# Kernel optimization log

Hardware: AMD Instinct MI355X
Metric: run time of the kernel (lower is better)

## Reference

```python
import jax, jax.numpy as jnp
import numpy as np
import math

EPS = 1e-5
ANGLES = [0, 30, 45, 60, 90, 135]
SIGMA = 0.3
POOL = 7  # top-hat neighbourhood


def make_masks(H, W):
    # Soft Gaussian stripe masks, one per angle: [A, H, W]
    ys = np.linspace(-1.0, 1.0, H)
    xs = np.linspace(-1.0, 1.0, W)
    gy, gx = np.meshgrid(ys, xs, indexing='ij')
    ms = []
    for a in ANGLES:
        t = a * math.pi / 180.0
        perp = gx * (-math.sin(t)) + gy * math.cos(t)
        ms.append(np.exp(-0.5 * (perp / SIGMA) ** 2))
    return jnp.asarray(np.stack(ms, axis=0), dtype=jnp.float32)


def dwconv1d(x, w):
    # x: [B, C, L], w: [C, 1, K] depthwise, 'same' padding (odd K)
    return jax.lax.conv_general_dilated(
        x, w, window_strides=(1,), padding='SAME',
        feature_group_count=x.shape[1],
        dimension_numbers=('NCH', 'OIH', 'NCH'))


def bn(x, gamma, beta, axes, pshape):
    # Training-mode batch norm (biased variance, as in torch forward)
    mean = x.mean(axes, keepdims=True)
    var = x.var(axes, keepdims=True)
    return (x - mean) * jax.lax.rsqrt(var + EPS) * gamma.reshape(pshape) + beta.reshape(pshape)


def maxpool_same(x, k):
    # torch MaxPool2d(k, stride=1, padding=k//2): pad with -inf
    p = k // 2
    return jax.lax.reduce_window(
        x, -jnp.inf, jax.lax.max,
        window_dimensions=(1, 1, k, k), window_strides=(1, 1, 1, 1),
        padding=[(0, 0), (0, 0), (p, p), (p, p)])


def setup_inputs() -> dict:
    key = jax.random.key(0)
    ks = jax.random.split(key, 8)
    B, C, H, W = 128, 576, 28, 28
    K = 3
    x = jax.random.normal(ks[0], (B, C, H, W), dtype=jnp.float32)
    h_w = jax.random.normal(ks[1], (C, 1, K), dtype=jnp.float32) * 0.2
    v_w = jax.random.normal(ks[2], (C, 1, K), dtype=jnp.float32) * 0.2
    f_w = jax.random.normal(ks[3], (C,), dtype=jnp.float32) * 0.2  # 1x1 dw conv = per-channel scale
    h_g = jnp.ones((C,), jnp.float32); h_b = jnp.zeros((C,), jnp.float32)
    v_g = jnp.ones((C,), jnp.float32); v_b = jnp.zeros((C,), jnp.float32)
    f_g = jnp.ones((C,), jnp.float32); f_b = jnp.zeros((C,), jnp.float32)
    return {"x": x, "h_w": h_w, "h_g": h_g, "h_b": h_b,
            "v_w": v_w, "v_g": v_g, "v_b": v_b,
            "f_w": f_w, "f_g": f_g, "f_b": f_b}


def reference(x, h_w, h_g, h_b, v_w, v_g, v_b, f_w, f_g, f_b):
    B, C, H, W = x.shape
    # Horizontal stream: mean over W -> dw conv1d over H -> BN1d -> sigmoid -> [B,C,H,1]
    ph = x.mean(axis=-1)                                   # [B, C, H]
    A_h = jax.nn.sigmoid(bn(dwconv1d(ph, h_w), h_g, h_b, (0, 2), (1, C, 1)))[..., None]
    # Vertical stream: mean over H -> dw conv1d over W -> BN1d -> sigmoid -> [B,C,1,W]
    pv = x.mean(axis=-2)                                   # [B, C, W]
    A_v = jax.nn.sigmoid(bn(dwconv1d(pv, v_w), v_g, v_b, (0, 2), (1, C, 1)))[:, :, None, :]
    # Focal spot stream: white top-hat -> per-channel scale -> BN2d -> sigmoid
    spots = maxpool_same(x, POOL) - x                      # [B, C, H, W]
    A_f = jax.nn.sigmoid(bn(spots * f_w[None, :, None, None], f_g, f_b, (0, 2, 3), (1, C, 1, 1)))
    # Orientation bank: masked global means, sigmoid per angle, mean over angles
    masks = make_masks(H, W)                               # [A, H, W]
    resp = jnp.einsum('bchw,ahw->bca', x, masks) / (H * W) # [B, C, A]
    A_t = jax.nn.sigmoid(resp).mean(axis=-1)[:, :, None, None]
    return x * A_h * A_v * A_f * A_t
```

## Files before the change

kernel.cpp:

```cpp
#include <hip/hip_runtime.h>
#include <math.h>

#define B 128
#define C 576
#define H 28
#define W 28
#define HW 784
#define NPLANE (B * C)
#define RMROWS 34
#define LOG2E 1.4426950408889634f

typedef float nfloat4 __attribute__((ext_vector_type(4)));

__device__ __forceinline__ float sigm2(float z2) { return 1.f / (1.f + exp2f(-z2)); }

__device__ __forceinline__ float4 fmax4(float4 a, float4 b) {
    a.x = fmaxf(a.x, b.x); a.y = fmaxf(a.y, b.y);
    a.z = fmaxf(a.z, b.z); a.w = fmaxf(a.w, b.w);
    return a;
}

__device__ __forceinline__ float4 hmax13(float4 Mv, float4 Lv, float4 Rv) {
    float mm   = fmaxf(fmaxf(Mv.x, Mv.y), fmaxf(Mv.z, Mv.w));
    float l23  = fmaxf(Lv.z, Lv.w);
    float l123 = fmaxf(Lv.y, l23);
    float r01  = fmaxf(Rv.x, Rv.y);
    float r012 = fmaxf(r01, Rv.z);
    float4 o;
    o.x = fmaxf(l123, mm);
    o.y = fmaxf(l23, fmaxf(mm, Rv.x));
    o.z = fmaxf(Lv.w, fmaxf(mm, r01));
    o.w = fmaxf(mm, r012);
    return o;
}

__device__ __forceinline__ float dpp_sum64(float v) {
    int t;
    t = __builtin_amdgcn_update_dpp(0, __float_as_int(v), 0x111, 0xf, 0xf, true);  v += __int_as_float(t);
    t = __builtin_amdgcn_update_dpp(0, __float_as_int(v), 0x112, 0xf, 0xf, true);  v += __int_as_float(t);
    t = __builtin_amdgcn_update_dpp(0, __float_as_int(v), 0x114, 0xf, 0xf, true);  v += __int_as_float(t);
    t = __builtin_amdgcn_update_dpp(0, __float_as_int(v), 0x118, 0xf, 0xf, true);  v += __int_as_float(t);
    t = __builtin_amdgcn_update_dpp(0, __float_as_int(v), 0x142, 0xa, 0xf, false); v += __int_as_float(t);
    t = __builtin_amdgcn_update_dpp(0, __float_as_int(v), 0x143, 0xc, 0xf, false); v += __int_as_float(t);
    return v;
}

__device__ __forceinline__ void wave_lds_fence() {
    asm volatile("s_waitcnt lgkmcnt(0)" ::: "memory");
    __builtin_amdgcn_sched_barrier(0);
}

__global__ void k0_init(float* __restrict__ masks, float* __restrict__ acc) {
    int idx = blockIdx.x * 256 + threadIdx.x;
    if (idx < 6 * C) acc[idx] = 0.f;
    if (idx < 6 * HW) {
        int a = idx / HW;
        int p = idx - a * HW;
        int r = p / W;
        int col = p - r * W;
        const float degs[6] = {0.f, 30.f, 45.f, 60.f, 90.f, 135.f};
        float t = degs[a] * 0.017453292519943295f;
        float gy = -1.f + r * (2.f / 27.f);
        float gx = -1.f + col * (2.f / 27.f);
        float perp = gx * (-sinf(t)) + gy * cosf(t);
        float z = perp * (1.f / 0.3f);
        masks[idx] = expf(-0.5f * z * z);
    }
}

__global__ __launch_bounds__(256, 7) void k1_stats(
    const float* __restrict__ x,
    const float* __restrict__ h_w, const float* __restrict__ v_w,
    const float* __restrict__ f_w, const float* __restrict__ masks,
    float* __restrict__ yh, float* __restrict__ yv,
    float* __restrict__ at, float* __restrict__ acc)
{
    const int tid = threadIdx.x;
    const int wvi = __builtin_amdgcn_readfirstlane(tid >> 6);
    const int l   = tid & 63;
    const int plane = blockIdx.x * 4 + wvi;
    const int c = plane % C;
    const float* xp = x + (size_t)plane * HW;

    __shared__ __align__(16) float uA[4][RMROWS * W];
    __shared__ __align__(16) float cpA[4][196];
    __shared__ __align__(16) float rpA[4][196];
    float* rm  = uA[wvi];
    float* sxv = rm + 3 * W;
    float* cp  = cpA[wvi];
    float* rp  = rpA[wvi];

    const int r0 = l / 7;
    const int u  = l - r0 * 7;
    const int q  = u * 4;
    const int qL = u ? q - 4 : 0;
    const int qR = (u < 6) ? q + 4 : 24;
    const bool act = (l < 49);

    const float4* mk0 = (const float4*)(masks);
    const float4* mk1 = (const float4*)(masks + HW);
    const float4* mk2 = (const float4*)(masks + 2 * HW);
    const float4* mk3 = (const float4*)(masks + 3 * HW);
    const float4* mk4 = (const float4*)(masks + 4 * HW);
    const float4* mk5 = (const float4*)(masks + 5 * HW);

    float4 Mv[4];
    float fs = 0.f, fss = 0.f;

    {
        float o0=0.f,o1=0.f,o2=0.f,o3=0.f,o4=0.f,o5=0.f;
        if (act) {
            float4 ca = make_float4(0.f, 0.f, 0.f, 0.f);
            float rw0, rw1, rw2, rw3;
            #pragma unroll
            for (int k = 0; k < 4; ++k) {
                const int unit = l + 49 * k;
                float4 v = ((const float4*)xp)[unit];
                Mv[k] = v;
                ((float4*)sxv)[unit] = v;
                ca.x += v.x; ca.y += v.y; ca.z += v.z; ca.w += v.w;
                float rs = (v.x + v.y) + (v.z + v.w);
                if (k == 0) rw0 = rs; else if (k == 1) rw1 = rs;
                else if (k == 2) rw2 = rs; else rw3 = rs;
                float4 m;
                m = mk0[unit]; o0 += v.x*m.x + v.y*m.y + v.z*m.z + v.w*m.w;
                m = mk1[unit]; o1 += v.x*m.x + v.y*m.y + v.z*m.z + v.w*m.w;
                m = mk2[unit]; o2 += v.x*m.x + v.y*m.y + v.z*m.z + v.w*m.w;
                m = mk3[unit]; o3 += v.x*m.x + v.y*m.y + v.z*m.z + v.w*m.w;
                m = mk4[unit]; o4 += v.x*m.x + v.y*m.y + v.z*m.z + v.w*m.w;
                m = mk5[unit]; o5 += v.x*m.x + v.y*m.y + v.z*m.z + v.w*m.w;
            }
            ((float4*)cp)[l] = ca;
            ((float4*)rp)[l] = make_float4(rw0, rw1, rw2, rw3);
        }
        o0 = dpp_sum64(o0); o1 = dpp_sum64(o1); o2 = dpp_sum64(o2);
        o3 = dpp_sum64(o3); o4 = dpp_sum64(o4); o5 = dpp_sum64(o5);
        if (l == 63) {
            const float s784 = LOG2E / (float)HW;
            float t = sigm2(o0 * s784) + sigm2(o1 * s784) + sigm2(o2 * s784)
                    + sigm2(o3 * s784) + sigm2(o4 * s784) + sigm2(o5 * s784);
            at[plane] = t * (1.f / 6.f);
        }
    }
    wave_lds_fence();

    if (act) {
        #pragma unroll
        for (int k = 0; k < 4; ++k) {
            const int r = r0 + 7 * k;
            const float* row = sxv + r * W;
            float4 Lv = *(const float4*)(row + qL);
            float4 Rv = *(const float4*)(row + qR);
            float4 hv = hmax13(Mv[k], Lv, Rv);
            *(float4*)(rm + (r + 3) * W + q) = hv;
            if (k == 0 && r0 == 0) {
                *(float4*)(rm + 0 * W + q) = hv;
                *(float4*)(rm + 1 * W + q) = hv;
                *(float4*)(rm + 2 * W + q) = hv;
            }
            if (k == 3 && r0 == 6) {
                *(float4*)(rm + 31 * W + q) = hv;
                *(float4*)(rm + 32 * W + q) = hv;
                *(float4*)(rm + 33 * W + q) = hv;
            }
        }
    }
    wave_lds_fence();

    if (act) {
        #pragma unroll
        for (int k = 0; k < 4; ++k) {
            const int r = r0 + 7 * k;
            const float* vb = rm + r * W + q;
            float4 m = *(const float4*)vb;
            m = fmax4(m, *(const float4*)(vb + W));
            m = fmax4(m, *(const float4*)(vb + 2 * W));
            m = fmax4(m, *(const float4*)(vb + 3 * W));
            m = fmax4(m, *(const float4*)(vb + 4 * W));
            m = fmax4(m, *(const float4*)(vb + 5 * W));
            m = fmax4(m, *(const float4*)(vb + 6 * W));
            float s0 = m.x - Mv[k].x;
            float s1 = m.y - Mv[k].y;
            float s2 = m.z - Mv[k].z;
            float s3 = m.w - Mv[k].w;
            fs  += (s0 + s1) + (s2 + s3);
            fss += (s0 * s0 + s1 * s1) + (s2 * s2 + s3 * s3);
        }
    }

    float ph_r = 0.f;
    float4 pvv = make_float4(0.f, 0.f, 0.f, 0.f);
    if (l < 28) {
        const int rr = l % 7, kk = l / 7;
        const float* rb = rp + rr * 28 + kk;
        float s = ((rb[0] + rb[4]) + (rb[8] + rb[12]))
                + ((rb[16] + rb[20]) + rb[24]);
        ph_r = s * (1.f / 28.f);
    }
    if (l < 7) {
        const float4* cb = (const float4*)cp;
        float4 a = cb[l];
        #pragma unroll
        for (int j = 1; j < 7; ++j) {
            float4 b = cb[l + 7 * j];
            a.x += b.x; a.y += b.y; a.z += b.z; a.w += b.w;
        }
        pvv.x = a.x * (1.f / 28.f); pvv.y = a.y * (1.f / 28.f);
        pvv.z = a.z * (1.f / 28.f); pvv.w = a.w * (1.f / 28.f);
    }

    const float hw0 = h_w[c * 3], hw1 = h_w[c * 3 + 1], hw2 = h_w[c * 3 + 2];
    float yhv = 0.f;
    {
        float pm = __shfl_up(ph_r, 1);
        float pp = __shfl_down(ph_r, 1);
        if (l < 28) {
            float a = (l > 0) ? pm : 0.f;
            float d = (l < 27) ? pp : 0.f;
            yhv = hw0 * a + hw1 * ph_r + hw2 * d;
            yh[(size_t)plane * H + l] = yhv;
        }
    }
    const float vw0 = v_w[c * 3], vw1 = v_w[c * 3 + 1], vw2 = v_w[c * 3 + 2];
    float yvs = 0.f, yvq = 0.f;
    {
        float lf = __shfl_up(pvv.w, 1);
        float rg = __shfl_down(pvv.x, 1);
        if (l < 7) {
            float a0 = (l > 0) ? lf : 0.f;
            float d3 = (l < 6) ? rg : 0.f;
            float4 y;
            y.x = vw0 * a0    + vw1 * pvv.x + vw2 * pvv.y;
            y.y = vw0 * pvv.x + vw1 * pvv.y + vw2 * pvv.z;
            y.z = vw0 * pvv.y + vw1 * pvv.z + vw2 * pvv.w;
            y.w = vw0 * pvv.z + vw1 * pvv.w + vw2 * d3;
            ((float4*)(yv + (size_t)plane * W))[l] = y;
            yvs = (y.x + y.y) + (y.z + y.w);
            yvq = (y.x * y.x + y.y * y.y) + (y.z * y.z + y.w * y.w);
        }
    }
    float yhq = yhv * yhv;

    fs = dpp_sum64(fs);  fss = dpp_sum64(fss);
    yhv = dpp_sum64(yhv); yhq = dpp_sum64(yhq);
    yvs = dpp_sum64(yvs); yvq = dpp_sum64(yvq);

    if (l == 63) {
        const float fwc = f_w[c];
        atomicAdd(&acc[0 * C + c], yhv);
        atomicAdd(&acc[1 * C + c], yhq);
        atomicAdd(&acc[2 * C + c], yvs);
        atomicAdd(&acc[3 * C + c], yvq);
        atomicAdd(&acc[4 * C + c], fs * fwc);
        atomicAdd(&acc[5 * C + c], fss * fwc * fwc);
    }
}

__global__ __launch_bounds__(64) void k2_params(
    const float* __restrict__ acc, const float* __restrict__ f_w,
    const float* __restrict__ hg, const float* __restrict__ hb,
    const float* __restrict__ vg, const float* __restrict__ vb,
    const float* __restrict__ fg, const float* __restrict__ fb,
    float* __restrict__ params)
{
    int c = blockIdx.x * 64 + threadIdx.x;
    if (c >= C) return;
    const float inv_nh = 1.f / (float)(B * H);
    const float inv_nf = 1.f / (float)(B * HW);
    float m, v, sc;
    m = acc[c] * inv_nh;
    v = acc[C + c] * inv_nh - m * m;
    sc = hg[c] * rsqrtf(v + 1e-5f);
    params[c * 8 + 0] = sc * LOG2E; params[c * 8 + 1] = (hb[c] - m * sc) * LOG2E;

    m = acc[2 * C + c] * inv_nh;
    v = acc[3 * C + c] * inv_nh - m * m;
    sc = vg[c] * rsqrtf(v + 1e-5f);
    params[c * 8 + 2] = sc * LOG2E; params[c * 8 + 3] = (vb[c] - m * sc) * LOG2E;

    m = acc[4 * C + c] * inv_nf;
    v = acc[5 * C + c] * inv_nf - m * m;
    sc = fg[c] * rsqrtf(v + 1e-5f);
    params[c * 8 + 4] = sc * f_w[c] * LOG2E;
    params[c * 8 + 5] = (fb[c] - m * sc) * LOG2E;
}

__global__ __launch_bounds__(256, 8) void k3_apply(
    const float* __restrict__ x,
    const float* __restrict__ yh, const float* __restrict__ yv,
    const float* __restrict__ at, const float* __restrict__ params,
    float* __restrict__ out)
{
    const int tid = threadIdx.x;
    const int wvi = __builtin_amdgcn_readfirstlane(tid >> 6);
    const int l   = tid & 63;
    const int plane = blockIdx.x * 4 + wvi;
    const int c = plane % C;
    const float* xp = x + (size_t)plane * HW;

    __shared__ __align__(16) float uA[4][RMROWS * W];
    float* rm  = uA[wvi];
    float* sxv = rm + 3 * W;

    const int r0 = l / 7;
    const int u  = l - r0 * 7;
    const int q  = u * 4;
    const int qL = u ? q - 4 : 0;
    const int qR = (u < 6) ? q + 4 : 24;
    const bool act = (l < 49);

    const float4 pA = *(const float4*)(params + c * 8);
    const float2 pB = *(const float2*)(params + c * 8 + 4);
    const float atv = at[plane];

    float4 Mv[4];

    if (act) {
        #pragma unroll
        for (int k = 0; k < 4; ++k) {
            const int unit = l + 49 * k;
            Mv[k] = ((const float4*)xp)[unit];
            ((float4*)sxv)[unit] = Mv[k];
        }
    }
    wave_lds_fence();

    if (act) {
        #pragma unroll
        for (int k = 0; k < 4; ++k) {
            const int r = r0 + 7 * k;
            const float* row = sxv + r * W;
            float4 Lv = *(const float4*)(row + qL);
            float4 Rv = *(const float4*)(row + qR);
            float4 hv = hmax13(Mv[k], Lv, Rv);
            *(float4*)(rm + (r + 3) * W + q) = hv;
            if (k == 0 && r0 == 0) {
                *(float4*)(rm + 0 * W + q) = hv;
                *(float4*)(rm + 1 * W + q) = hv;
                *(float4*)(rm + 2 * W + q) = hv;
            }
            if (k == 3 && r0 == 6) {
                *(float4*)(rm + 31 * W + q) = hv;
                *(float4*)(rm + 32 * W + q) = hv;
                *(float4*)(rm + 33 * W + q) = hv;
            }
        }
    }
    wave_lds_fence();

    if (act) {
        float4 yv4 = ((const float4*)(yv + (size_t)plane * W))[u];
        float4 av;
        av.x = sigm2(pA.z * yv4.x + pA.w);
        av.y = sigm2(pA.z * yv4.y + pA.w);
        av.z = sigm2(pA.z * yv4.z + pA.w);
        av.w = sigm2(pA.z * yv4.w + pA.w);
        nfloat4* op = (nfloat4*)(out + (size_t)plane * HW);
        #pragma unroll
        for (int k = 0; k < 4; ++k) {
            const int r = r0 + 7 * k;
            const float* vb = rm + r * W + q;
            float4 m = *(const float4*)vb;
            m = fmax4(m, *(const float4*)(vb + W));
            m = fmax4(m, *(const float4*)(vb + 2 * W));
            m = fmax4(m, *(const float4*)(vb + 3 * W));
            m = fmax4(m, *(const float4*)(vb + 4 * W));
            m = fmax4(m, *(const float4*)(vb + 5 * W));
            m = fmax4(m, *(const float4*)(vb + 6 * W));
            float ahk = sigm2(pA.x * yh[(size_t)plane * H + r] + pA.y) * atv;
            nfloat4 o;
            o.x = Mv[k].x * ahk * av.x * sigm2(fmaf(pB.x, m.x, fmaf(-pB.x, Mv[k].x, pB.y)));
            o.y = Mv[k].y * ahk * av.y * sigm2(fmaf(pB.x, m.y, fmaf(-pB.x, Mv[k].y, pB.y)));
            o.z = Mv[k].z * ahk * av.z * sigm2(fmaf(pB.x, m.z, fmaf(-pB.x, Mv[k].z, pB.y)));
            o.w = Mv[k].w * ahk * av.w * sigm2(fmaf(pB.x, m.w, fmaf(-pB.x, Mv[k].w, pB.y)));
            __builtin_nontemporal_store(o, &op[l + 49 * k]);
        }
    }
}

extern "C" void kernel_launch(void* const* d_in, const int* in_sizes, int n_in,
                              void* d_out, int out_size, void* d_ws, size_t ws_size,
                              hipStream_t stream) {
    const float* x   = (const float*)d_in[0];
    const float* h_w = (const float*)d_in[1];
    const float* h_g = (const float*)d_in[2];
    const float* h_b = (const float*)d_in[3];
    const float* v_w = (const float*)d_in[4];
    const float* v_g = (const float*)d_in[5];
    const float* v_b = (const float*)d_in[6];
    const float* f_w = (const float*)d_in[7];
    const float* f_g = (const float*)d_in[8];
    const float* f_b = (const float*)d_in[9];
    float* out = (float*)d_out;
    float* ws = (float*)d_ws;

    float* masks  = ws;
    float* acc    = ws + 4704;
    float* params = ws + 8160;
    float* at     = ws + 12768;
    float* yh     = ws + 86496;
    float* yv     = ws + 2150880;

    k0_init<<<19, 256, 0, stream>>>(masks, acc);
    k1_stats<<<NPLANE / 4, 256, 0, stream>>>(x, h_w, v_w, f_w, masks, yh, yv, at, acc);
    k2_params<<<9, 64, 0, stream>>>(acc, f_w, h_g, h_b, v_g, v_b, f_g, f_b, params);
    k3_apply<<<NPLANE / 4, 256, 0, stream>>>(x, yh, yv, at, params, out);
}
```

Measured before the change: 191.8 us.

## Derive 0/90-degree orientation responses from row/column sums and use fp16 dot masks

New measurement: 176.5 us. -8.0%, faster.

```diff
diff --git a/kernel.cpp b/kernel.cpp
--- a/kernel.cpp
+++ b/kernel.cpp
@@ -11,6 +11,7 @@
 #define LOG2E 1.4426950408889634f
 
 typedef float nfloat4 __attribute__((ext_vector_type(4)));
+typedef _Float16 half2v __attribute__((ext_vector_type(2)));
 
 __device__ __forceinline__ float sigm2(float z2) { return 1.f / (1.f + exp2f(-z2)); }
 
@@ -50,28 +51,41 @@
     __builtin_amdgcn_sched_barrier(0);
 }
 
-__global__ void k0_init(float* __restrict__ masks, float* __restrict__ acc) {
+__device__ __forceinline__ float dot4h(half2v vlo, half2v vhi, uint2 md, float acc) {
+    half2v mlo = __builtin_bit_cast(half2v, md.x);
+    half2v mhi = __builtin_bit_cast(half2v, md.y);
+#if __has_builtin(__builtin_amdgcn_fdot2)
+    acc = __builtin_amdgcn_fdot2(vlo, mlo, acc, false);
+    acc = __builtin_amdgcn_fdot2(vhi, mhi, acc, false);
+#else
+    acc += (float)vlo.x * (float)mlo.x + (float)vlo.y * (float)mlo.y
+         + (float)vhi.x * (float)mhi.x + (float)vhi.y * (float)mhi.y;
+#endif
+    return acc;
+}
+
+__global__ void k0_init(_Float16* __restrict__ masksf16, float* __restrict__ acc) {
     int idx = blockIdx.x * 256 + threadIdx.x;
     if (idx < 6 * C) acc[idx] = 0.f;
-    if (idx < 6 * HW) {
+    if (idx < 4 * HW) {
         int a = idx / HW;
         int p = idx - a * HW;
         int r = p / W;
         int col = p - r * W;
-        const float degs[6] = {0.f, 30.f, 45.f, 60.f, 90.f, 135.f};
+        const float degs[4] = {30.f, 45.f, 60.f, 135.f};
         float t = degs[a] * 0.017453292519943295f;
         float gy = -1.f + r * (2.f / 27.f);
         float gx = -1.f + col * (2.f / 27.f);
         float perp = gx * (-sinf(t)) + gy * cosf(t);
         float z = perp * (1.f / 0.3f);
-        masks[idx] = expf(-0.5f * z * z);
+        masksf16[idx] = (_Float16)expf(-0.5f * z * z);
     }
 }
 
 __global__ __launch_bounds__(256, 7) void k1_stats(
     const float* __restrict__ x,
     const float* __restrict__ h_w, const float* __restrict__ v_w,
-    const float* __restrict__ f_w, const float* __restrict__ masks,
+    const float* __restrict__ f_w, const _Float16* __restrict__ masksf16,
     float* __restrict__ yh, float* __restrict__ yv,
     float* __restrict__ at, float* __restrict__ acc)
 {
@@ -97,50 +111,32 @@
     const int qR = (u < 6) ? q + 4 : 24;
     const bool act = (l < 49);
 
-    const float4* mk0 = (const float4*)(masks);
-    const float4* mk1 = (const float4*)(masks + HW);
-    const float4* mk2 = (const float4*)(masks + 2 * HW);
-    const float4* mk3 = (const float4*)(masks + 3 * HW);
-    const float4* mk4 = (const float4*)(masks + 4 * HW);
-    const float4* mk5 = (const float4*)(masks + 5 * HW);
+    const uint2* mk2p = (const uint2*)masksf16;
 
     float4 Mv[4];
     float fs = 0.f, fss = 0.f;
-
-    {
-        float o0=0.f,o1=0.f,o2=0.f,o3=0.f,o4=0.f,o5=0.f;
-        if (act) {
-            float4 ca = make_float4(0.f, 0.f, 0.f, 0.f);
-            float rw0, rw1, rw2, rw3;
-            #pragma unroll
-            for (int k = 0; k < 4; ++k) {
-                const int unit = l + 49 * k;
-                float4 v = ((const float4*)xp)[unit];
-                Mv[k] = v;
-                ((float4*)sxv)[unit] = v;
-                ca.x += v.x; ca.y += v.y; ca.z += v.z; ca.w += v.w;
-                float rs = (v.x + v.y) + (v.z + v.w);
-                if (k == 0) rw0 = rs; else if (k == 1) rw1 = rs;
-                else if (k == 2) rw2 = rs; else rw3 = rs;
-                float4 m;
-                m = mk0[unit]; o0 += v.x*m.x + v.y*m.y + v.z*m.z + v.w*m.w;
-                m = mk1[unit]; o1 += v.x*m.x + v.y*m.y + v.z*m.z + v.w*m.w;
-                m = mk2[unit]; o2 += v.x*m.x + v.y*m.y + v.z*m.z + v.w*m.w;
-                m = mk3[unit]; o3 += v.x*m.x + v.y*m.y + v.z*m.z + v.w*m.w;
-                m = mk4[unit]; o4 += v.x*m.x + v.y*m.y + v.z*m.z + v.w*m.w;
-                m = mk5[unit]; o5 += v.x*m.x + v.y*m.y + v.z*m.z + v.w*m.w;
-            }
-            ((float4*)cp)[l] = ca;
-            ((float4*)rp)[l] = make_float4(rw0, rw1, rw2, rw3);
-        }
-        o0 = dpp_sum64(o0); o1 = dpp_sum64(o1); o2 = dpp_sum64(o2);
-        o3 = dpp_sum64(o3); o4 = dpp_sum64(o4); o5 = dpp_sum64(o5);
-        if (l == 63) {
-            const float s784 = LOG2E / (float)HW;
-            float t = sigm2(o0 * s784) + sigm2(o1 * s784) + sigm2(o2 * s784)
-                    + sigm2(o3 * s784) + sigm2(o4 * s784) + sigm2(o5 * s784);
-            at[plane] = t * (1.f / 6.f);
-        }
+    float o30 = 0.f, o45 = 0.f, o60 = 0.f, o135 = 0.f;
+
+    if (act) {
+        float4 ca = make_float4(0.f, 0.f, 0.f, 0.f);
+        float rw[4];
+        #pragma unroll
+        for (int k = 0; k < 4; ++k) {
+            const int unit = l + 49 * k;
+            float4 v = ((const float4*)xp)[unit];
+            Mv[k] = v;
+            ((float4*)sxv)[unit] = v;
+            ca.x += v.x; ca.y += v.y; ca.z += v.z; ca.w += v.w;
+            rw[k] = (v.x + v.y) + (v.z + v.w);
+            half2v vlo = __builtin_bit_cast(half2v, __builtin_amdgcn_cvt_pkrtz(v.x, v.y));
+            half2v vhi = __builtin_bit_cast(half2v, __builtin_amdgcn_cvt_pkrtz(v.z, v.w));
+            o30  = dot4h(vlo, vhi, mk2p[unit],           o30);
+            o45  = dot4h(vlo, vhi, mk2p[196 + unit],     o45);
+            o60  = dot4h(vlo, vhi, mk2p[2 * 196 + unit], o60);
+            o135 = dot4h(vlo, vhi, mk2p[3 * 196 + unit], o135);
+        }
+        ((float4*)cp)[l] = ca;
+        ((float4*)rp)[l] = make_float4(rw[0], rw[1], rw[2], rw[3]);
     }
     wave_lds_fence();
 
@@ -188,26 +184,21 @@
         }
     }
 
-    float ph_r = 0.f;
-    float4 pvv = make_float4(0.f, 0.f, 0.f, 0.f);
+    float s_row = 0.f, colsum = 0.f, ph_r = 0.f;
     if (l < 28) {
         const int rr = l % 7, kk = l / 7;
         const float* rb = rp + rr * 28 + kk;
-        float s = ((rb[0] + rb[4]) + (rb[8] + rb[12]))
-                + ((rb[16] + rb[20]) + rb[24]);
-        ph_r = s * (1.f / 28.f);
-    }
-    if (l < 7) {
-        const float4* cb = (const float4*)cp;
-        float4 a = cb[l];
-        #pragma unroll
-        for (int j = 1; j < 7; ++j) {
-            float4 b = cb[l + 7 * j];
-            a.x += b.x; a.y += b.y; a.z += b.z; a.w += b.w;
-        }
-        pvv.x = a.x * (1.f / 28.f); pvv.y = a.y * (1.f / 28.f);
-        pvv.z = a.z * (1.f / 28.f); pvv.w = a.w * (1.f / 28.f);
-    }
+        s_row = ((rb[0] + rb[4]) + (rb[8] + rb[12]))
+              + ((rb[16] + rb[20]) + rb[24]);
+        ph_r = s_row * (1.f / 28.f);
+        colsum = ((cp[l] + cp[l + 28]) + (cp[l + 56] + cp[l + 84]))
+               + ((cp[l + 112] + cp[l + 140]) + cp[l + 168]);
+    }
+
+    float g = -1.f + (float)l * (2.f / 27.f);
+    float mg = exp2f(-8.014972687f * g * g);
+    float r0s  = (l < 28) ? s_row  * mg : 0.f;
+    float r90s = (l < 28) ? colsum * mg : 0.f;
 
     const float hw0 = h_w[c * 3], hw1 = h_w[c * 3 + 1], hw2 = h_w[c * 3 + 2];
     float yhv = 0.f;
@@ -222,30 +213,33 @@
         }
     }
     const float vw0 = v_w[c * 3], vw1 = v_w[c * 3 + 1], vw2 = v_w[c * 3 + 2];
-    float yvs = 0.f, yvq = 0.f;
+    float yvv = 0.f;
     {
-        float lf = __shfl_up(pvv.w, 1);
-        float rg = __shfl_down(pvv.x, 1);
-        if (l < 7) {
-            float a0 = (l > 0) ? lf : 0.f;
-            float d3 = (l < 6) ? rg : 0.f;
-            float4 y;
-            y.x = vw0 * a0    + vw1 * pvv.x + vw2 * pvv.y;
-            y.y = vw0 * pvv.x + vw1 * pvv.y + vw2 * pvv.z;
-            y.z = vw0 * pvv.y + vw1 * pvv.z + vw2 * pvv.w;
-            y.w = vw0 * pvv.z + vw1 * pvv.w + vw2 * d3;
-            ((float4*)(yv + (size_t)plane * W))[l] = y;
-            yvs = (y.x + y.y) + (y.z + y.w);
-            yvq = (y.x * y.x + y.y * y.y) + (y.z * y.z + y.w * y.w);
+        float pvm = colsum * (1.f / 28.f);
+        float pm2 = __shfl_up(pvm, 1);
+        float pp2 = __shfl_down(pvm, 1);
+        if (l < 28) {
+            float a = (l > 0) ? pm2 : 0.f;
+            float d = (l < 27) ? pp2 : 0.f;
+            yvv = vw0 * a + vw1 * pvm + vw2 * d;
+            yv[(size_t)plane * W + l] = yvv;
         }
     }
     float yhq = yhv * yhv;
-
-    fs = dpp_sum64(fs);  fss = dpp_sum64(fss);
-    yhv = dpp_sum64(yhv); yhq = dpp_sum64(yhq);
-    yvs = dpp_sum64(yvs); yvq = dpp_sum64(yvq);
+    float yvq = yvv * yvv;
+
+    fs  = dpp_sum64(fs);   fss  = dpp_sum64(fss);
+    yhv = dpp_sum64(yhv);  yhq  = dpp_sum64(yhq);
+    float yvs = dpp_sum64(yvv); yvq = dpp_sum64(yvq);
+    o30 = dpp_sum64(o30);  o45  = dpp_sum64(o45);
+    o60 = dpp_sum64(o60);  o135 = dpp_sum64(o135);
+    r0s = dpp_sum64(r0s);  r90s = dpp_sum64(r90s);
 
     if (l == 63) {
+        const float s784 = LOG2E / (float)HW;
+        float t = sigm2(r0s * s784) + sigm2(o30 * s784) + sigm2(o45 * s784)
+                + sigm2(o60 * s784) + sigm2(r90s * s784) + sigm2(o135 * s784);
+        at[plane] = t * (1.f / 6.f);
         const float fwc = f_w[c];
         atomicAdd(&acc[0 * C + c], yhv);
         atomicAdd(&acc[1 * C + c], yhq);
@@ -349,7 +343,11 @@
     wave_lds_fence();
 
     if (act) {
-        float4 yv4 = ((const float4*)(yv + (size_t)plane * W))[u];
+        float4 yv4;
+        yv4.x = yv[(size_t)plane * W + q];
+        yv4.y = yv[(size_t)plane * W + q + 1];
+        yv4.z = yv[(size_t)plane * W + q + 2];
+        yv4.w = yv[(size_t)plane * W + q + 3];
         float4 av;
         av.x = sigm2(pA.z * yv4.x + pA.w);
         av.y = sigm2(pA.z * yv4.y + pA.w);
@@ -394,15 +392,15 @@
     float* out = (float*)d_out;
     float* ws = (float*)d_ws;
 
-    float* masks  = ws;
-    float* acc    = ws + 4704;
-    float* params = ws + 8160;
-    float* at     = ws + 12768;
-    float* yh     = ws + 86496;
-    float* yv     = ws + 2150880;
-
-    k0_init<<<19, 256, 0, stream>>>(masks, acc);
-    k1_stats<<<NPLANE / 4, 256, 0, stream>>>(x, h_w, v_w, f_w, masks, yh, yv, at, acc);
+    _Float16* masksf16 = (_Float16*)ws;
+    float* acc    = ws + 1568;
+    float* params = ws + 5024;
+    float* at     = ws + 9632;
+    float* yh     = ws + 83360;
+    float* yv     = ws + 2147744;
+
+    k0_init<<<14, 256, 0, stream>>>(masksf16, acc);
+    k1_stats<<<NPLANE / 4, 256, 0, stream>>>(x, h_w, v_w, f_w, masksf16, yh, yv, at, acc);
     k2_params<<<9, 64, 0, stream>>>(acc, f_w, h_g, h_b, v_g, v_b, f_g, f_b, params);
     k3_apply<<<NPLANE / 4, 256, 0, stream>>>(x, yh, yv, at, params, out);
 }
```
